# Performance work log

Hardware: AMD Instinct MI355X
Metric: run time of the kernel (lower is better)

The kernel has to match this reference:

```python
import jax, jax.numpy as jnp
import numpy as np
import math

B, S, T = 32, 128, 64
FEAT = 16
H = 1024
V = 32000


def _gru_step(x, h, wih, whh, bih, bhh):
    # torch nn.GRU cell: gates ordered (r, z, n)
    gi = x @ wih.T + bih
    gh = h @ whh.T + bhh
    ir, iz, in_ = jnp.split(gi, 3, axis=-1)
    hr, hz, hn = jnp.split(gh, 3, axis=-1)
    r = jax.nn.sigmoid(ir + hr)
    z = jax.nn.sigmoid(iz + hz)
    n = jnp.tanh(in_ + r * hn)
    return (1.0 - z) * n + z * h


def _forward(features, target_tokens, temp_W, temp_b, hum_W, hum_b, cloud_W, cloud_b,
             time_W, time_b, other_W, other_b, fi_W, fi_b,
             enc_wih, enc_whh, enc_bih, enc_bhh, emb, attn_W, attn_b,
             dec_wih, dec_whh, dec_bih, dec_bhh, out_W, out_b):
    b = features.shape[0]
    # per-feature projections (dropout = identity in eval mode)
    temp = features[:, :, 0:1] @ temp_W.T + temp_b
    hum = features[:, :, 1:2] @ hum_W.T + hum_b
    cloud = features[:, :, 2:3] @ cloud_W.T + cloud_b
    time = features[:, :, -5:-3] @ time_W.T + time_b
    other_in = jnp.concatenate([features[:, :, 3:-5], features[:, :, -3:]], axis=2)
    other = other_in @ other_W.T + other_b
    concat = jnp.concatenate([temp, hum, cloud, time, other], axis=2)  # [B,S,2H]
    proj = jnp.tanh(concat @ fi_W.T + fi_b)  # [B,S,H]

    # encoder GRU over time
    def enc_step(h, x):
        h2 = _gru_step(x, h, enc_wih, enc_whh, enc_bih, enc_bhh)
        return h2, h2
    h0 = jnp.zeros((b, H), proj.dtype)
    h_last, enc_outs = jax.lax.scan(enc_step, h0, proj.transpose(1, 0, 2))
    enc_out = enc_outs.transpose(1, 0, 2)  # [B,S,H]

    # attention keys computed once (loop-invariant in the original)
    keys = enc_out @ attn_W.T + attn_b  # [B,S,H]
    scale = 1.0 / math.sqrt(H)

    # decoder: teacher_forcing_ratio = 1.0 -> input at step t is target_tokens[:, t-1]
    def dec_step(h, tok):
        e = emb[tok]  # [B,H]
        scores = jnp.einsum('bh,bsh->bs', h, keys) * scale
        w = jax.nn.softmax(scores, axis=-1)
        ctx = jnp.einsum('bs,bsh->bh', w, enc_out)
        x = jnp.concatenate([e, ctx], axis=-1)  # [B,2H]
        h2 = _gru_step(x, h, dec_wih, dec_whh, dec_bih, dec_bhh)
        pred = jnp.concatenate([h2, ctx], axis=-1) @ out_W.T + out_b  # [B,V]
        return h2, pred

    _, preds = jax.lax.scan(dec_step, h_last, target_tokens[:, :-1].T)  # [T-1,B,V]
    outputs = jnp.zeros((b, target_tokens.shape[1], V), preds.dtype)
    outputs = outputs.at[:, 0, target_tokens[0, 0]].set(1.0)
    outputs = outputs.at[:, 1:, :].set(preds.transpose(1, 0, 2))
    return outputs


def setup_inputs() -> dict:
    key = jax.random.key(0)
    ks = jax.random.split(key, 32)
    nrm = lambda k, sh: jax.random.normal(k, sh, jnp.float32) * 0.05
    Hq = H // 4
    d = {}
    d['features'] = jax.random.normal(ks[0], (B, S, FEAT), jnp.float32)
    d['target_tokens'] = jax.random.randint(ks[1], (B, T), 0, V, dtype=jnp.int32)
    d['temp_W'] = nrm(ks[2], (Hq, 1)); d['temp_b'] = nrm(ks[3], (Hq,))
    d['hum_W'] = nrm(ks[4], (Hq, 1)); d['hum_b'] = nrm(ks[5], (Hq,))
    d['cloud_W'] = nrm(ks[6], (Hq, 1)); d['cloud_b'] = nrm(ks[7], (Hq,))
    d['time_W'] = nrm(ks[8], (Hq, 2)); d['time_b'] = nrm(ks[9], (Hq,))
    d['other_W'] = nrm(ks[10], (H, FEAT - 5)); d['other_b'] = nrm(ks[11], (H,))
    d['fi_W'] = nrm(ks[12], (H, 2 * H)); d['fi_b'] = nrm(ks[13], (H,))
    d['enc_wih'] = nrm(ks[14], (3 * H, H)); d['enc_whh'] = nrm(ks[15], (3 * H, H))
    d['enc_bih'] = nrm(ks[16], (3 * H,)); d['enc_bhh'] = nrm(ks[17], (3 * H,))
    d['emb'] = nrm(ks[18], (V, H))
    d['attn_W'] = nrm(ks[19], (H, H)); d['attn_b'] = nrm(ks[20], (H,))
    d['dec_wih'] = nrm(ks[21], (3 * H, 2 * H)); d['dec_whh'] = nrm(ks[22], (3 * H, H))
    d['dec_bih'] = nrm(ks[23], (3 * H,)); d['dec_bhh'] = nrm(ks[24], (3 * H,))
    d['out_W'] = nrm(ks[25], (V, 2 * H)); d['out_b'] = nrm(ks[26], (V,))
    return d


def reference(features, target_tokens, temp_W, temp_b, hum_W, hum_b, cloud_W, cloud_b,
              time_W, time_b, other_W, other_b, fi_W, fi_b,
              enc_wih, enc_whh, enc_bih, enc_bhh, emb, attn_W, attn_b,
              dec_wih, dec_whh, dec_bih, dec_bhh, out_W, out_b):
    return _forward(features, target_tokens, temp_W, temp_b, hum_W, hum_b, cloud_W, cloud_b,
                    time_W, time_b, other_W, other_b, fi_W, fi_b,
                    enc_wih, enc_whh, enc_bih, enc_bhh, emb, attn_W, attn_b,
                    dec_wih, dec_whh, dec_bih, dec_bhh, out_W, out_b)
```

## Files before the change

kernel.cpp:

```cpp
#include <hip/hip_runtime.h>

typedef float f32x4 __attribute__((ext_vector_type(4)));
typedef __bf16 bf16x8 __attribute__((ext_vector_type(8)));

#define DI static __device__ __forceinline__

DI unsigned short f2bf(float f) {
  unsigned u = __float_as_uint(f);
  u = (u + 0x7fffu + ((u >> 16) & 1u)) >> 16;
  return (unsigned short)u;
}
DI unsigned pk2(float lo, float hi) {
  return (unsigned)f2bf(lo) | ((unsigned)f2bf(hi) << 16);
}
DI float bflo(unsigned u) { return __uint_as_float(u << 16); }
DI float bfhi(unsigned u) { return __uint_as_float(u & 0xffff0000u); }
DI float sigm(float x) { return 1.0f / (1.0f + expf(-x)); }

DI void gl_lds16(const unsigned short* g, unsigned short* l) {
  __builtin_amdgcn_global_load_lds(
      (const __attribute__((address_space(1))) unsigned int*)g,
      (__attribute__((address_space(3))) unsigned int*)l, 16, 0, 0);
}

DI void st64_sc1(unsigned long long* p, unsigned long long v) {
  __hip_atomic_store(p, v, __ATOMIC_RELAXED, __HIP_MEMORY_SCOPE_AGENT);
}
DI int ldw(const int* p) {
  return __hip_atomic_load(p, __ATOMIC_RELAXED, __HIP_MEMORY_SCOPE_AGENT);
}
DI void stw(int* p, int v) {
  __hip_atomic_store(p, v, __ATOMIC_RELAXED, __HIP_MEMORY_SCOPE_AGENT);
}

DI void burn4(int n) {
  float x0 = 1.f + (float)(int)threadIdx.x, x1 = 2.f, x2 = 3.f, x3 = 4.f;
#pragma unroll 1
  for (int i = 0; i < n; ++i) {
    x0 = __builtin_fmaf(x0, 1.0000001f, 1e-9f);
    x1 = __builtin_fmaf(x1, 1.0000001f, 2e-9f);
    x2 = __builtin_fmaf(x2, 1.0000001f, 3e-9f);
    x3 = __builtin_fmaf(x3, 1.0000001f, 4e-9f);
  }
  asm volatile("" :: "v"(x0), "v"(x1), "v"(x2), "v"(x3));
}

DI void waitrel2(const int* relbase, int repl, int target) {
  const int* w = relbase + repl * 32;
  while (ldw(w) < target) burn4(40);
  asm volatile("" ::: "memory");
}
DI void arrive_release(int* cnt, int nblk, int* relbase, int relval) {
  if (threadIdx.x == 0) {
    int old = __hip_atomic_fetch_add(cnt, 1, __ATOMIC_RELAXED, __HIP_MEMORY_SCOPE_AGENT);
    if (old == nblk - 1) {
#pragma unroll
      for (int i = 0; i < 8; ++i) stw(relbase + i * 32, relval);
    }
  }
}

__global__ void k_fold(const float* __restrict__ tW, const float* __restrict__ tb,
                       const float* __restrict__ hW, const float* __restrict__ hb,
                       const float* __restrict__ cW, const float* __restrict__ cb,
                       const float* __restrict__ tiW, const float* __restrict__ tib,
                       const float* __restrict__ oW, const float* __restrict__ ob,
                       const float* __restrict__ fiW, const float* __restrict__ fib,
                       float* __restrict__ M, float* __restrict__ b0v)
{
  int g = blockIdx.x * 256 + threadIdx.x;
  if (g >= 1024 * 17) return;
  int h = g / 17, f = g - h * 17;
  const float* fw = fiW + (size_t)h * 2048;
  float s = 0.f;
  if (f == 16) {
    for (int k = 0; k < 256; ++k) s += fw[k] * tb[k];
    for (int k = 0; k < 256; ++k) s += fw[256 + k] * hb[k];
    for (int k = 0; k < 256; ++k) s += fw[512 + k] * cb[k];
    for (int k = 0; k < 256; ++k) s += fw[768 + k] * tib[k];
    for (int r = 0; r < 1024; ++r) s += fw[1024 + r] * ob[r];
    b0v[h] = s + fib[h];
  } else if (f == 0) {
    for (int k = 0; k < 256; ++k) s += fw[k] * tW[k];
    M[h * 16 + 0] = s;
  } else if (f == 1) {
    for (int k = 0; k < 256; ++k) s += fw[256 + k] * hW[k];
    M[h * 16 + 1] = s;
  } else if (f == 2) {
    for (int k = 0; k < 256; ++k) s += fw[512 + k] * cW[k];
    M[h * 16 + 2] = s;
// ... 108 lines not shown
    gl_lds16(ga1 + kt, &As[(tid + 256) * 8]);
    gl_lds16(gb0 + kt, &Bs[tid * 8]);
    gl_lds16(gb1 + kt, &Bs[(tid + 256) * 8]);
    __syncthreads();
    bf16x8 af[4], bfv[4];
#pragma unroll
    for (int m = 0; m < 4; ++m) af[m] = *(const bf16x8*)&As[(wm + m * 16 + lr) * 32 + lkb];
#pragma unroll
    for (int n = 0; n < 4; ++n) bfv[n] = *(const bf16x8*)&Bs[(wn + n * 16 + lr) * 32 + lkb];
#pragma unroll
    for (int m = 0; m < 4; ++m)
#pragma unroll
      for (int n = 0; n < 4; ++n)
        acc[m][n] = __builtin_amdgcn_mfma_f32_16x16x32_bf16(af[m], bfv[n], acc[m][n], 0, 0, 0);
  }

#pragma unroll
  for (int m = 0; m < 4; ++m) {
    int rb = tm * 128 + wm + m * 16 + ((lane >> 4) << 2);
#pragma unroll
    for (int n = 0; n < 4; ++n) {
      int c = tn * 128 + wn + n * 16 + lr;
      float bb = bias[c];
#pragma unroll
      for (int i = 0; i < 4; ++i) {
        float v = acc[m][n][i] + bb;
        int r = rb + i;
        if (MODE == 0) {
          Cf[(size_t)r * ldc + c] = v;
        } else if (MODE == 1) {
          Cb[(size_t)r * ldc + c] = f2bf(v);
        } else if (MODE == 3) {
          Cb[(size_t)c * 4096 + r] = f2bf(v);
        } else {
          if (r < 2016) {
            int t = r >> 5, b2 = r & 31;
            Cf[((size_t)b2 * 64 + t + 1) * 32000 + coloff + c] = v;
          }
        }
      }
    }
  }
}

__global__ __launch_bounds__(256, 1)
void k_enc_scan(const float* __restrict__ gi_all, const float* __restrict__ whh,
                const float* __restrict__ bhh, float* __restrict__ hfp,
                unsigned short* __restrict__ enc_bf,
                int* __restrict__ cntE, int* __restrict__ relE)
{
  const int tid = threadIdx.x;
  const int blk = blockIdx.x;

  __shared__ unsigned short W[48 * 1024];
  __shared__ float Cred[4 * 2 * 3 * 64 * 4];
  const int lane = tid & 63, wave = tid >> 6;
  const int j0 = blk * 16;
  const int repl = blk & 7;

  for (int i = tid; i < 48 * 128; i += 256) {
    int r = i >> 7, c = i & 127;
    int gr = ((r >> 4) << 10) + j0 + (r & 15);
    const float* src = whh + ((size_t)gr << 10) + (c << 3);
    f32x4 a = *(const f32x4*)src, b = *(const f32x4*)(src + 4);
    uint4 o;
    o.x = pk2(a[0], a[1]); o.y = pk2(a[2], a[3]);
    o.z = pk2(b[0], b[1]); o.w = pk2(b[2], b[3]);
    *(uint4*)&W[(r << 10) + ((c ^ (r & 7)) << 3)] = o;
  }
  __syncthreads();

// ... 58 lines not shown

    float h2v[2];
#pragma unroll
    for (int cc = 0; cc < 2; ++cc) {
      int lj = clb[cc] + cj[cc], reg = creg[cc], m = cm[cc];
      float Cr = 0.f, Cz = 0.f, Cn = 0.f;
#pragma unroll
      for (int w = 0; w < 4; ++w) {
        Cr += Cred[((((w * 2 + m) * 3 + 0) * 64 + lj) << 2) + reg];
        Cz += Cred[((((w * 2 + m) * 3 + 1) * 64 + lj) << 2) + reg];
        Cn += Cred[((((w * 2 + m) * 3 + 2) * 64 + lj) << 2) + reg];
      }
      float r = sigm(gp[cc][0] + Cr + bh0[cc]);
      float z = sigm(gp[cc][1] + Cz + bh1[cc]);
      float n = tanhf(gp[cc][2] + r * (Cn + bh2[cc]));
      float h2 = (1.f - z) * n + z * hp[cc];
      h2v[cc] = h2; hp[cc] = h2;
    }
    if (s == 127) {
      hfp[cb[0] * 1024 + j0 + cj[0]] = h2v[0];
      hfp[cb[1] * 1024 + j0 + cj[1]] = h2v[1];
    }
#pragma unroll
    for (int cc = 0; cc < 2; ++cc) {
      unsigned short sv = f2bf(h2v[cc]);
      unsigned p = (unsigned)sv | (((unsigned)__shfl_xor((int)(unsigned)sv, 1)) << 16);
      unsigned q = (unsigned)__shfl_xor((int)p, 2);
      if ((tid & 3) == 0) {
        unsigned long long dv = (unsigned long long)p | ((unsigned long long)q << 32);
        st64_sc1((unsigned long long*)&enc_bf[((size_t)cb[cc] * 128 + s) * 1024 + j0 + cj[cc]], dv);
      }
    }
    __syncthreads();
    arrive_release(&cntE[s << 4], 64, relE, s + 1);
  }
}

__global__ __launch_bounds__(256, 1)
void k_dec_scan(const float* __restrict__ gi_e, const float* __restrict__ whh,
                const float* __restrict__ bhh,
                const unsigned short* __restrict__ keys,
                const unsigned short* __restrict__ enc_bf,
                unsigned short* __restrict__ hcat, const float* __restrict__ hfp0,
                const unsigned short* __restrict__ xeT, float* __restrict__ w_all,
                int* __restrict__ cntW, int* __restrict__ cntH,
                int* __restrict__ relDe, int* __restrict__ relDh)
{
  static __shared__ __attribute__((aligned(16))) char smem[135168];
  const int tid = threadIdx.x;
  const int blk = blockIdx.x;
  const int repl = blk & 7;

  if (blk < 64) {
    unsigned short* Ks = (unsigned short*)smem;
    unsigned short* hsh = (unsigned short*)(smem + 131072);
    float* parr = (float*)(smem + 133120);
    const int b = blk >> 1, half = blk & 1;
    const int lane = tid & 63, wave = tid >> 6;

    for (int i = tid; i < 64 * 128; i += 256) {
      int s = i >> 7, c = i & 127;
      uint4 kv = *(const uint4*)(keys + ((size_t)(b * 128 + half * 64 + s) << 10) + (c << 3));
      *(uint4*)&Ks[(s << 10) + ((c ^ (s & 7)) << 3)] = kv;
    }
    __syncthreads();

#pragma unroll 1
    for (int t = 0; t < 63; ++t) {
      if (t) waitrel2(relDh, repl, t);
      const unsigned short* hsrc = (t == 0)
          ? (enc_bf + (size_t)b * 131072 + (size_t)127 * 1024)
          : (hcat + ((size_t)(t - 1) * 32 + b) * 2048);
      *(uint2*)&hsh[tid * 4] = *(const uint2*)(hsrc + tid * 4);
      float a0 = 0.f, a1 = 0.f;
#pragma unroll 8
      for (int i = 0; i < 32; i += 2) {
        int c0 = wave * 32 + i, c1 = c0 + 1;
        uint4 kv0 = *(const uint4*)&Ks[(lane << 10) + ((c0 ^ (lane & 7)) << 3)];
        uint4 kv1 = *(const uint4*)&Ks[(lane << 10) + ((c1 ^ (lane & 7)) << 3)];
        uint4 hv0 = *(const uint4*)&hsh[c0 << 3];
        uint4 hv1 = *(const uint4*)&hsh[c1 << 3];
        a0 += bflo(kv0.x) * bflo(hv0.x) + bfhi(kv0.x) * bfhi(hv0.x)
            + bflo(kv0.y) * bflo(hv0.y) + bfhi(kv0.y) * bfhi(hv0.y)
            + bflo(kv0.z) * bflo(hv0.z) + bfhi(kv0.z) * bfhi(hv0.z)
            + bflo(kv0.w) * bflo(hv0.w) + bfhi(kv0.w) * bfhi(hv0.w);
        a1 += bflo(kv1.x) * bflo(hv1.x) + bfhi(kv1.x) * bfhi(hv1.x)
            + bflo(kv1.y) * bflo(hv1.y) + bfhi(kv1.y) * bfhi(hv1.y)
            + bflo(kv1.z) * bflo(hv1.z) + bfhi(kv1.z) * bfhi(hv1.z)
            + bflo(kv1.w) * bflo(hv1.w) + bfhi(kv1.w) * bfhi(hv1.w);
      }
      parr[wave * 64 + lane] = a0 + a1;
      __syncthreads();
      if (tid < 64) {
        float sc = (parr[tid] + parr[64 + tid] + parr[128 + tid] + parr[192 + tid]) * 0.03125f;
        float e = expf(sc);
        float eo = __shfl_xor(e, 1);
        if ((tid & 1) == 0) {
          unsigned long long dv = (unsigned long long)__float_as_uint(e)
                                | ((unsigned long long)__float_as_uint(eo) << 32);
          st64_sc1((unsigned long long*)(w_all + ((size_t)t * 32 + b) * 128 + half * 64 + tid), dv);
        }
      }
      __syncthreads();
      arrive_release(&cntW[t << 4], 64, relDe, t + 1);
    }
    return;
  }

  unsigned short* Wh = (unsigned short*)smem;
  float* Cred = (float*)(smem + 65536);
  const int lane = tid & 63, wave = tid >> 6;
  const int gblk = blk - 64;
  const int j0 = gblk * 8;

  for (int i = tid; i < 32 * 128; i += 256) {
    int r = i >> 7, c = i & 127;
    int off = (r << 10) + ((c ^ (r & 7)) << 3);
    uint4 oh;
    oh.x = oh.y = oh.z = oh.w = 0u;
    if (r < 24) {
      int gr = ((r >> 3) << 10) + j0 + (r & 7);
      const float* sh = whh + ((size_t)gr << 10) + (c << 3);
      f32x4 a = *(const f32x4*)sh, b = *(const f32x4*)(sh + 4);
      oh.x = pk2(a[0], a[1]); oh.y = pk2(a[2], a[3]);
      oh.z = pk2(b[0], b[1]); oh.w = pk2(b[2], b[3]);
    }
    *(uint4*)&Wh[off] = oh;
  }
  __syncthreads();

  const int gb = tid >> 3, gj = tid & 7;
  const int glb = ((gb & 15) >> 2) * 16;
  const int greg = gb & 3, gm = gb >> 4;
  const float bh0 = bhh[j0 + gj];
  const float bh1 = bhh[1024 + j0 + gj];
  const float bh2 = bhh[2048 + j0 + gj];
  float hpv = hfp0[gb * 1024 + j0 + gj];

  uint4 x0v[16], x1v[16], x2v[16];
  {
    const unsigned short* x0 = xeT + ((size_t)(j0 + gj) << 12) + gb * 128;
    const unsigned short* x1 = xeT + ((size_t)(1024 + j0 + gj) << 12) + gb * 128;
    const unsigned short* x2 = xeT + ((size_t)(2048 + j0 + gj) << 12) + gb * 128;
#pragma unroll
    for (int i = 0; i < 16; ++i) {
      x0v[i] = *(const uint4*)(x0 + i * 8);
      x1v[i] = *(const uint4*)(x1 + i * 8);
      x2v[i] = *(const uint4*)(x2 + i * 8);
    }
  }

#pragma unroll 1
  for (int t = 0; t < 63; ++t) {
    const float* gie = gi_e + ((size_t)t * 32 + gb) * 3072 + j0 + gj;
    float g0 = gie[0], g1 = gie[1024], g2 = gie[2048];

    if (t) waitrel2(relDh, repl, t);
    const unsigned short* abase;
    size_t astr;
    if (t == 0) { abase = enc_bf + (size_t)127 * 1024; astr = 131072; }
    else { abase = hcat + (size_t)(t - 1) * 32 * 2048; astr = 2048; }
    const int k0 = wave << 8;
    f32x4 acc[2][2];
#pragma unroll
    for (int m = 0; m < 2; ++m)
#pragma unroll
      for (int n = 0; n < 2; ++n) { acc[m][n][0]=0.f; acc[m][n][1]=0.f; acc[m][n][2]=0.f; acc[m][n][3]=0.f; }
    {
      bf16x8 af[2][8];
#pragma unroll
      for (int kk = 0; kk < 8; ++kk) {
        int k = k0 + kk * 32 + ((lane >> 4) << 3);
        af[0][kk] = *(const bf16x8*)(abase + (size_t)(lane & 15) * astr + k);
        af[1][kk] = *(const bf16x8*)(abase + (size_t)(16 + (lane & 15)) * astr + k);
      }
#pragma unroll
      for (int kk = 0; kk < 8; ++kk) {
        int c = ((k0 + kk * 32) >> 3) + (lane >> 4);
#pragma unroll
        for (int n = 0; n < 2; ++n) {
          int wr = n * 16 + (lane & 15);
          bf16x8 bfr = *(const bf16x8*)&Wh[(wr << 10) + ((c ^ (wr & 7)) << 3)];
          acc[0][n] = __builtin_amdgcn_mfma_f32_16x16x32_bf16(af[0][kk], bfr, acc[0][n], 0, 0, 0);
          acc[1][n] = __builtin_amdgcn_mfma_f32_16x16x32_bf16(af[1][kk], bfr, acc[1][n], 0, 0, 0);
        }
      }
    }
#pragma unroll
    for (int m = 0; m < 2; ++m)
#pragma unroll
      for (int n = 0; n < 2; ++n)
        *(f32x4*)&Cred[((((wave * 2 + m) * 2 + n) * 64) + lane) << 2] = acc[m][n];
    __syncthreads();

    waitrel2(relDe, repl, t + 1);
    const float* wrow = w_all + ((size_t)t * 32 + gb) * 128;
    float se = 0.f, cx0 = 0.f, cx1 = 0.f, cx2 = 0.f;
#pragma unroll
    for (int i = 0; i < 16; ++i) {
      f32x4 wa = *(const f32x4*)(wrow + i * 8);
      f32x4 wb2 = *(const f32x4*)(wrow + i * 8 + 4);
      se += (wa[0] + wa[1]) + (wa[2] + wa[3]) + (wb2[0] + wb2[1]) + (wb2[2] + wb2[3]);
      uint4 a0 = x0v[i], a1 = x1v[i], a2 = x2v[i];
      cx0 += wa[0]*bflo(a0.x) + wa[1]*bfhi(a0.x) + wa[2]*bflo(a0.y) + wa[3]*bfhi(a0.y)
           + wb2[0]*bflo(a0.z) + wb2[1]*bfhi(a0.z) + wb2[2]*bflo(a0.w) + wb2[3]*bfhi(a0.w);
      cx1 += wa[0]*bflo(a1.x) + wa[1]*bfhi(a1.x) + wa[2]*bflo(a1.y) + wa[3]*bfhi(a1.y)
           + wb2[0]*bflo(a1.z) + wb2[1]*bfhi(a1.z) + wb2[2]*bflo(a1.w) + wb2[3]*bfhi(a1.w);
      cx2 += wa[0]*bflo(a2.x) + wa[1]*bfhi(a2.x) + wa[2]*bflo(a2.y) + wa[3]*bfhi(a2.y)
           + wb2[0]*bflo(a2.z) + wb2[1]*bfhi(a2.z) + wb2[2]*bflo(a2.w) + wb2[3]*bfhi(a2.w);
    }
    float inv = 1.f / se;
    cx0 *= inv; cx1 *= inv; cx2 *= inv;

    {
      float Chr = 0.f, Chz = 0.f, Chn = 0.f;
#pragma unroll
      for (int w = 0; w < 4; ++w) {
        Chr += Cred[((((w * 2 + gm) * 2 + 0) * 64 + glb + gj) << 2) + greg];
        Chz += Cred[((((w * 2 + gm) * 2 + 0) * 64 + glb + gj + 8) << 2) + greg];
        Chn += Cred[((((w * 2 + gm) * 2 + 1) * 64 + glb + gj) << 2) + greg];
      }
      float r = sigm(g0 + cx0 + Chr + bh0);
      float z = sigm(g1 + cx1 + Chz + bh1);
      float n2 = tanhf(g2 + cx2 + r * (Chn + bh2));
      float h2 = (1.f - z) * n2 + z * hpv;
      hpv = h2;
      unsigned short sv = f2bf(h2);
      unsigned p = (unsigned)sv | (((unsigned)__shfl_xor((int)(unsigned)sv, 1)) << 16);
      unsigned q = (unsigned)__shfl_xor((int)p, 2);
      if ((tid & 3) == 0) {
        unsigned long long dv = (unsigned long long)p | ((unsigned long long)q << 32);
        st64_sc1((unsigned long long*)&hcat[((size_t)t * 32 + gb) * 2048 + j0 + gj], dv);
      }
    }
    __syncthreads();
    arrive_release(&cntH[t << 4], 128, relDh, t + 1);
  }
}

__global__ __launch_bounds__(256)
void k_ctx(const float* __restrict__ w_all, const unsigned short* __restrict__ enc_bf,
           unsigned short* __restrict__ hcat)
{
  __shared__ float wsh[8][128];
  __shared__ float inv[8];
  const int b = blockIdx.x, tg = blockIdx.y;
  const int t0 = tg * 8;
  const int nt = (t0 + 8 <= 63) ? 8 : (63 - t0);
  const int tid = threadIdx.x;
  for (int idx = tid; idx < 8 * 128; idx += 256) {
    int tt = idx >> 7, s = idx & 127;
    wsh[tt][s] = (tt < nt) ? w_all[((size_t)(t0 + tt) * 32 + b) * 128 + s] : 0.f;
  }
  __syncthreads();
  if (tid < 8) {
    float s = 0.f;
    for (int i = 0; i < 128; ++i) s += wsh[tid][i];
    inv[tid] = (tid < nt) ? 1.f / s : 0.f;
  }
  __syncthreads();
  const int j0 = tid * 4;
  f32x4 cacc[8];
#pragma unroll
  for (int tt = 0; tt < 8; ++tt) { cacc[tt][0]=0.f; cacc[tt][1]=0.f; cacc[tt][2]=0.f; cacc[tt][3]=0.f; }
  const unsigned short* eb = enc_bf + ((size_t)b << 17) + j0;
  for (int s = 0; s < 128; ++s) {
    uint2 ev = *(const uint2*)(eb + ((size_t)s << 10));
    float v0 = bflo(ev.x), v1 = bfhi(ev.x), v2 = bflo(ev.y), v3 = bfhi(ev.y);
#pragma unroll
    for (int tt = 0; tt < 8; ++tt) {
      float w = wsh[tt][s];
      cacc[tt][0] += w * v0; cacc[tt][1] += w * v1;
      cacc[tt][2] += w * v2; cacc[tt][3] += w * v3;
    }
  }
#pragma unroll
  for (int tt = 0; tt < 8; ++tt) {
    if (tt < nt) {
      float iv = inv[tt];
      uint2 co;
      co.x = pk2(cacc[tt][0] * iv, cacc[tt][1] * iv);
      co.y = pk2(cacc[tt][2] * iv, cacc[tt][3] * iv);
      *(uint2*)(hcat + ((size_t)(t0 + tt) * 32 + b) * 2048 + 1024 + j0) = co;
    }
  }
}

extern "C" void kernel_launch(void* const* d_in, const int* in_sizes, int n_in,
                              void* d_out, int out_size, void* d_ws, size_t ws_size,
                              hipStream_t stream)
{
  const float* features = (const float*)d_in[0];
  const int*   toks     = (const int*)d_in[1];
  const float* temp_W = (const float*)d_in[2];  const float* temp_b = (const float*)d_in[3];
  const float* hum_W  = (const float*)d_in[4];  const float* hum_b  = (const float*)d_in[5];
  const float* cloud_W= (const float*)d_in[6];  const float* cloud_b= (const float*)d_in[7];
  const float* time_W = (const float*)d_in[8];  const float* time_b = (const float*)d_in[9];
  const float* other_W= (const float*)d_in[10]; const float* other_b= (const float*)d_in[11];
  const float* fi_W   = (const float*)d_in[12]; const float* fi_b   = (const float*)d_in[13];
  const float* enc_wih= (const float*)d_in[14]; const float* enc_whh= (const float*)d_in[15];
  const float* enc_bih= (const float*)d_in[16]; const float* enc_bhh= (const float*)d_in[17];
  const float* emb    = (const float*)d_in[18];
  const float* attn_W = (const float*)d_in[19]; const float* attn_b = (const float*)d_in[20];
  const float* dec_wih= (const float*)d_in[21]; const float* dec_whh= (const float*)d_in[22];
  const float* dec_bih= (const float*)d_in[23]; const float* dec_bhh= (const float*)d_in[24];
  const float* out_W  = (const float*)d_in[25]; const float* out_b  = (const float*)d_in[26];
  float* out = (float*)d_out;
  char* ws = (char*)d_ws;

  int*            cntE    = (int*)(ws + 0);
  int*            cntW    = (int*)(ws + 8192);
  int*            cntH    = (int*)(ws + 12288);
  int*            relE    = (int*)(ws + 16384);
  int*            relDe   = (int*)(ws + 17408);
  int*            relDh   = (int*)(ws + 18432);
  float*          zbias   = (float*)(ws + 20480);
  float*          Mf      = (float*)(ws + 32768);
  float*          b0v     = (float*)(ws + 98304);
  float*          hfp     = (float*)(ws + 102400);
  unsigned short* hcat    = (unsigned short*)(ws + 233472);
  unsigned short* keys_bf = (unsigned short*)(ws + 8622080);
  unsigned short* enc_bf  = (unsigned short*)(ws + 17010688);
  float*          w_all   = (float*)(ws + 25399296);
  float*          gi_e    = (float*)(ws + 26447872);
  unsigned short* xeT     = (unsigned short*)(ws + 51613696);
  float*          gi_all  = (float*)(ws + 76779520);
  unsigned short* proj_bf = (unsigned short*)(ws + 127111168);
  unsigned short* e_bf    = (unsigned short*)(ws + 135499776);
  unsigned short* wihE_bf = (unsigned short*)(ws + 139694080);
  unsigned short* attnW_bf= (unsigned short*)(ws + 145985536);
  unsigned short* wihD_bf = (unsigned short*)(ws + 148082688);
  unsigned short* wihDc_bf= (unsigned short*)(ws + 154374144);
  unsigned short* outW_bf = (unsigned short*)(ws + 26447872);

  hipMemsetAsync(ws, 0, 32768, stream);
  hipMemsetAsync(ws + 233472 + (size_t)2016 * 2048 * 2, 0, 32 * 2048 * 2, stream);

  k_conv<<<1536, 256, 0, stream>>>(enc_wih, wihE_bf, 393216);
  k_conv<<<512, 256, 0, stream>>>(attn_W, attnW_bf, 131072);
  k_conv_str<<<3072, 256, 0, stream>>>(dec_wih, wihD_bf, 0);
  k_conv_str<<<3072, 256, 0, stream>>>(dec_wih, wihDc_bf, 1024);

  k_fold<<<68, 256, 0, stream>>>(temp_W, temp_b, hum_W, hum_b, cloud_W, cloud_b,
                                 time_W, time_b, other_W, other_b, fi_W, fi_b, Mf, b0v);
  k_proj<<<dim3(4096, 4), 256, 0, stream>>>(features, Mf, b0v, proj_bf);

  gemm_bf<0><<<768, 256, 0, stream>>>(proj_bf, wihE_bf, enc_bih, gi_all, nullptr,
                                      32, 1024, 1024, 1024, 3072, 0);
  k_enc_scan<<<64, 256, 0, stream>>>(gi_all, enc_whh, enc_bhh, hfp, enc_bf, cntE, relE);

  gemm_bf<1><<<256, 256, 0, stream>>>(enc_bf, attnW_bf, attn_b, nullptr, keys_bf,
                                      32, 1024, 1024, 1024, 1024, 0);
  k_gather_e<<<2048, 256, 0, stream>>>(toks, emb, e_bf);
  gemm_bf<0><<<384, 256, 0, stream>>>(e_bf, wihD_bf, dec_bih, gi_e, nullptr,
                                      16, 1024, 1024, 1024, 3072, 0);
  gemm_bf<3><<<768, 256, 0, stream>>>(enc_bf, wihDc_bf, zbias, nullptr, xeT,
                                      32, 1024, 1024, 1024, 0, 0);
  k_dec_scan<<<192, 256, 0, stream>>>(gi_e, dec_whh, dec_bhh, keys_bf, enc_bf,
                                      hcat, hfp, xeT, w_all, cntW, cntH, relDe, relDh);
  k_ctx<<<dim3(32, 8), 256, 0, stream>>>(w_all, enc_bf, hcat);

  k_conv<<<2048, 256, 0, stream>>>(out_W, outW_bf, 4096000);
  gemm_bf<2><<<2000, 256, 0, stream>>>(hcat, outW_bf, out_b, out, nullptr,
                                       16, 2048, 2048, 2048, 0, 0);
  k_conv<<<2048, 256, 0, stream>>>(out_W + (size_t)16000 * 2048, outW_bf, 4096000);
  gemm_bf<2><<<2000, 256, 0, stream>>>(hcat, outW_bf, out_b + 16000, out, nullptr,
                                       16, 2048, 2048, 2048, 0, 16000);
  k_onehot<<<4000, 256, 0, stream>>>(toks, out);
}
```

Before: 2.752 ms.

## Fuse context and output projection into persistent decoder scan kernel

The decoder scan becomes a persistent kernel with four roles: attention-score blocks (now 128, each handling 32 source positions), GRU hidden-state blocks, per-batch context blocks that write ctx into hcat every step, and output-projection blocks that convert out_W panels to bf16 and run MFMA tiles as soon as the needed timesteps are released. This removes the separate k_ctx, conversion and output GEMM launches and overlaps the large vocab projection with the sequential recurrence. The cost is more release counters and flags (32 replicas), spin-waiting output blocks that compete for CUs, and a dependence on all 413 blocks being co-resident to avoid deadlock.

```diff
diff --git a/kernel.cpp b/kernel.cpp
--- a/kernel.cpp
+++ b/kernel.cpp
@@ -50,12 +50,12 @@
   while (ldw(w) < target) burn4(40);
   asm volatile("" ::: "memory");
 }
-DI void arrive_release(int* cnt, int nblk, int* relbase, int relval) {
+DI void arrive_release(int* cnt, int nblk, int* relbase, int relval, int nrep) {
   if (threadIdx.x == 0) {
     int old = __hip_atomic_fetch_add(cnt, 1, __ATOMIC_RELAXED, __HIP_MEMORY_SCOPE_AGENT);
     if (old == nblk - 1) {
-#pragma unroll
-      for (int i = 0; i < 8; ++i) stw(relbase + i * 32, relval);
+#pragma unroll 1
+      for (int i = 0; i < nrep; ++i) stw(relbase + i * 32, relval);
     }
   }
 }
@@ -230,11 +230,60 @@
           Cb[(size_t)r * ldc + c] = f2bf(v);
         } else if (MODE == 3) {
           Cb[(size_t)c * 4096 + r] = f2bf(v);
-        } else {
-          if (r < 2016) {
-            int t = r >> 5, b2 = r & 31;
-            Cf[((size_t)b2 * 64 + t + 1) * 32000 + coloff + c] = v;
-          }
+        }
+      }
+    }
+  }
+}
+
+DI void out_tile(const unsigned short* A, const unsigned short* Bp,
+                 const float* out_b, float* out, int rowbase, int colbase,
+                 unsigned short* As, unsigned short* Bs, int tid)
+{
+  const int lane = tid & 63, wave = tid >> 6;
+  const int wm = (wave & 1) << 6, wn = (wave >> 1) << 6;
+  const int r0 = tid >> 2, kc0 = (tid & 3) << 3;
+  const unsigned short* ga0 = A + (size_t)r0 * 2048 + kc0;
+  const unsigned short* ga1 = A + (size_t)(64 + r0) * 2048 + kc0;
+  const unsigned short* gb0 = Bp + (size_t)r0 * 2048 + kc0;
+  const unsigned short* gb1 = Bp + (size_t)(64 + r0) * 2048 + kc0;
+  const int lr = lane & 15, lkb = (lane >> 4) << 3;
+  f32x4 acc[4][4];
+#pragma unroll
+  for (int m = 0; m < 4; ++m)
+#pragma unroll
+    for (int n = 0; n < 4; ++n) { acc[m][n][0]=0.f; acc[m][n][1]=0.f; acc[m][n][2]=0.f; acc[m][n][3]=0.f; }
+  for (int kt = 0; kt < 2048; kt += 32) {
+    __syncthreads();
+    gl_lds16(ga0 + kt, &As[tid * 8]);
+    gl_lds16(ga1 + kt, &As[(tid + 256) * 8]);
+    gl_lds16(gb0 + kt, &Bs[tid * 8]);
+    gl_lds16(gb1 + kt, &Bs[(tid + 256) * 8]);
+    __syncthreads();
+    bf16x8 af[4], bfv[4];
+#pragma unroll
+    for (int m = 0; m < 4; ++m) af[m] = *(const bf16x8*)&As[(wm + m * 16 + lr) * 32 + lkb];
+#pragma unroll
+    for (int n = 0; n < 4; ++n) bfv[n] = *(const bf16x8*)&Bs[(wn + n * 16 + lr) * 32 + lkb];
+#pragma unroll
+    for (int m = 0; m < 4; ++m)
+#pragma unroll
+      for (int n = 0; n < 4; ++n)
+        acc[m][n] = __builtin_amdgcn_mfma_f32_16x16x32_bf16(af[m], bfv[n], acc[m][n], 0, 0, 0);
+  }
+#pragma unroll
+  for (int m = 0; m < 4; ++m) {
+    int rb = rowbase + wm + m * 16 + ((lane >> 4) << 2);
+#pragma unroll
+    for (int n = 0; n < 4; ++n) {
+      int cg = colbase + wn + n * 16 + lr;
+      float bb = out_b[cg];
+#pragma unroll
+      for (int i = 0; i < 4; ++i) {
+        int r = rb + i;
+        if (r < 2016) {
+          int t = r >> 5, b2 = r & 31;
+          out[((size_t)b2 * 64 + t + 1) * 32000 + cg] = acc[m][n][i] + bb;
         }
       }
     }
@@ -359,7 +408,7 @@
       }
     }
     __syncthreads();
-    arrive_release(&cntE[s << 4], 64, relE, s + 1);
+    arrive_release(&cntE[s << 4], 64, relE, s + 1, 8);
   }
 }
 
@@ -370,25 +419,29 @@
                 const unsigned short* __restrict__ enc_bf,
                 unsigned short* __restrict__ hcat, const float* __restrict__ hfp0,
                 const unsigned short* __restrict__ xeT, float* __restrict__ w_all,
-                int* __restrict__ cntW, int* __restrict__ cntH,
-                int* __restrict__ relDe, int* __restrict__ relDh)
-{
-  static __shared__ __attribute__((aligned(16))) char smem[135168];
+                int* __restrict__ cntW, int* __restrict__ cntH, int* __restrict__ cntC,
+                int* __restrict__ relDe, int* __restrict__ relDh, int* __restrict__ relCtx,
+                const float* __restrict__ out_W, const float* __restrict__ out_b,
+                unsigned short* __restrict__ outWp, float* __restrict__ out)
+{
+  static __shared__ __attribute__((aligned(16))) char smem[81920];
   const int tid = threadIdx.x;
   const int blk = blockIdx.x;
-  const int repl = blk & 7;
-
-  if (blk < 64) {
+  const int repl = blk & 31;
+
+  if (blk < 128) {
     unsigned short* Ks = (unsigned short*)smem;
-    unsigned short* hsh = (unsigned short*)(smem + 131072);
-    float* parr = (float*)(smem + 133120);
-    const int b = blk >> 1, half = blk & 1;
+    unsigned short* hsh = (unsigned short*)(smem + 65536);
+    float* parr = (float*)(smem + 67584);
+    const int b = blk >> 2, q = blk & 3;
     const int lane = tid & 63, wave = tid >> 6;
-
-    for (int i = tid; i < 64 * 128; i += 256) {
-      int s = i >> 7, c = i & 127;
-      uint4 kv = *(const uint4*)(keys + ((size_t)(b * 128 + half * 64 + s) << 10) + (c << 3));
-      *(uint4*)&Ks[(s << 10) + ((c ^ (s & 7)) << 3)] = kv;
+    const int s = lane & 31;
+    const int ksl = (wave << 1) | (lane >> 5);
+
+    for (int i = tid; i < 32 * 128; i += 256) {
+      int sr = i >> 7, c = i & 127;
+      uint4 kv = *(const uint4*)(keys + ((size_t)(b * 128 + q * 32 + sr) << 10) + (c << 3));
+      *(uint4*)&Ks[(sr << 10) + ((c ^ (sr & 15)) << 3)] = kv;
     }
     __syncthreads();
 
@@ -399,12 +452,13 @@
           ? (enc_bf + (size_t)b * 131072 + (size_t)127 * 1024)
           : (hcat + ((size_t)(t - 1) * 32 + b) * 2048);
       *(uint2*)&hsh[tid * 4] = *(const uint2*)(hsrc + tid * 4);
+      __syncthreads();
       float a0 = 0.f, a1 = 0.f;
-#pragma unroll 8
-      for (int i = 0; i < 32; i += 2) {
-        int c0 = wave * 32 + i, c1 = c0 + 1;
-        uint4 kv0 = *(const uint4*)&Ks[(lane << 10) + ((c0 ^ (lane & 7)) << 3)];
-        uint4 kv1 = *(const uint4*)&Ks[(lane << 10) + ((c1 ^ (lane & 7)) << 3)];
+#pragma unroll
+      for (int i = 0; i < 16; i += 2) {
+        int c0 = (ksl << 4) + i, c1 = c0 + 1;
+        uint4 kv0 = *(const uint4*)&Ks[(s << 10) + ((c0 ^ (s & 15)) << 3)];
+        uint4 kv1 = *(const uint4*)&Ks[(s << 10) + ((c1 ^ (s & 15)) << 3)];
         uint4 hv0 = *(const uint4*)&hsh[c0 << 3];
         uint4 hv1 = *(const uint4*)&hsh[c1 << 3];
         a0 += bflo(kv0.x) * bflo(hv0.x) + bfhi(kv0.x) * bfhi(hv0.x)
@@ -416,199 +470,217 @@
             + bflo(kv1.z) * bflo(hv1.z) + bfhi(kv1.z) * bfhi(hv1.z)
             + bflo(kv1.w) * bflo(hv1.w) + bfhi(kv1.w) * bfhi(hv1.w);
       }
-      parr[wave * 64 + lane] = a0 + a1;
-      __syncthreads();
-      if (tid < 64) {
-        float sc = (parr[tid] + parr[64 + tid] + parr[128 + tid] + parr[192 + tid]) * 0.03125f;
-        float e = expf(sc);
+      parr[(ksl << 5) + s] = a0 + a1;
+      __syncthreads();
+      if (tid < 32) {
+        float sc = 0.f;
+#pragma unroll
+        for (int k = 0; k < 8; ++k) sc += parr[(k << 5) + tid];
+        float e = expf(sc * 0.03125f);
         float eo = __shfl_xor(e, 1);
         if ((tid & 1) == 0) {
           unsigned long long dv = (unsigned long long)__float_as_uint(e)
                                 | ((unsigned long long)__float_as_uint(eo) << 32);
-          st64_sc1((unsigned long long*)(w_all + ((size_t)t * 32 + b) * 128 + half * 64 + tid), dv);
+          st64_sc1((unsigned long long*)(w_all + ((size_t)t * 32 + b) * 128 + q * 32 + tid), dv);
         }
       }
       __syncthreads();
-      arrive_release(&cntW[t << 4], 64, relDe, t + 1);
+      arrive_release(&cntW[t << 4], 128, relDe, t + 1, 32);
     }
     return;
   }
 
-  unsigned short* Wh = (unsigned short*)smem;
-  float* Cred = (float*)(smem + 65536);
-  const int lane = tid & 63, wave = tid >> 6;
-  const int gblk = blk - 64;
-  const int j0 = gblk * 8;
-
-  for (int i = tid; i < 32 * 128; i += 256) {
-    int r = i >> 7, c = i & 127;
-    int off = (r << 10) + ((c ^ (r & 7)) << 3);
-    uint4 oh;
-    oh.x = oh.y = oh.z = oh.w = 0u;
-    if (r < 24) {
-      int gr = ((r >> 3) << 10) + j0 + (r & 7);
-      const float* sh = whh + ((size_t)gr << 10) + (c << 3);
-      f32x4 a = *(const f32x4*)sh, b = *(const f32x4*)(sh + 4);
-      oh.x = pk2(a[0], a[1]); oh.y = pk2(a[2], a[3]);
-      oh.z = pk2(b[0], b[1]); oh.w = pk2(b[2], b[3]);
-    }
-    *(uint4*)&Wh[off] = oh;
-  }
-  __syncthreads();
-
-  const int gb = tid >> 3, gj = tid & 7;
-  const int glb = ((gb & 15) >> 2) * 16;
-  const int greg = gb & 3, gm = gb >> 4;
-  const float bh0 = bhh[j0 + gj];
-  const float bh1 = bhh[1024 + j0 + gj];
-  const float bh2 = bhh[2048 + j0 + gj];
-  float hpv = hfp0[gb * 1024 + j0 + gj];
-
-  uint4 x0v[16], x1v[16], x2v[16];
+  if (blk < 256) {
+    unsigned short* Wh = (unsigned short*)smem;
+    float* Cred = (float*)(smem + 65536);
+    const int lane = tid & 63, wave = tid >> 6;
+    const int gblk = blk - 128;
+    const int j0 = gblk * 8;
+
+    for (int i = tid; i < 32 * 128; i += 256) {
+      int r = i >> 7, c = i & 127;
+      int off = (r << 10) + ((c ^ (r & 7)) << 3);
+      uint4 oh;
+      oh.x = oh.y = oh.z = oh.w = 0u;
+      if (r < 24) {
+        int gr = ((r >> 3) << 10) + j0 + (r & 7);
+        const float* sh = whh + ((size_t)gr << 10) + (c << 3);
+        f32x4 a = *(const f32x4*)sh, b = *(const f32x4*)(sh + 4);
+        oh.x = pk2(a[0], a[1]); oh.y = pk2(a[2], a[3]);
+        oh.z = pk2(b[0], b[1]); oh.w = pk2(b[2], b[3]);
+      }
+      *(uint4*)&Wh[off] = oh;
+    }
+    __syncthreads();
+
+    const int gb = tid >> 3, gj = tid & 7;
+    const int glb = ((gb & 15) >> 2) * 16;
+    const int greg = gb & 3, gm = gb >> 4;
+    const float bh0 = bhh[j0 + gj];
+    const float bh1 = bhh[1024 + j0 + gj];
+    const float bh2 = bhh[2048 + j0 + gj];
+    float hpv = hfp0[gb * 1024 + j0 + gj];
+
+    uint4 x0v[16], x1v[16], x2v[16];
+    {
+      const unsigned short* x0 = xeT + ((size_t)(j0 + gj) << 12) + gb * 128;
+      const unsigned short* x1 = xeT + ((size_t)(1024 + j0 + gj) << 12) + gb * 128;
+      const unsigned short* x2 = xeT + ((size_t)(2048 + j0 + gj) << 12) + gb * 128;
+#pragma unroll
+      for (int i = 0; i < 16; ++i) {
+        x0v[i] = *(const uint4*)(x0 + i * 8);
+        x1v[i] = *(const uint4*)(x1 + i * 8);
+        x2v[i] = *(const uint4*)(x2 + i * 8);
+      }
+    }
+
+#pragma unroll 1
+    for (int t = 0; t < 63; ++t) {
+      const float* gie = gi_e + ((size_t)t * 32 + gb) * 3072 + j0 + gj;
+      float g0 = gie[0], g1 = gie[1024], g2 = gie[2048];
+
+      if (t) waitrel2(relDh, repl, t);
+      const unsigned short* abase;
+      size_t astr;
+      if (t == 0) { abase = enc_bf + (size_t)127 * 1024; astr = 131072; }
+      else { abase = hcat + (size_t)(t - 1) * 32 * 2048; astr = 2048; }
+      const int k0 = wave << 8;
+      f32x4 acc[2][2];
+#pragma unroll
+      for (int m = 0; m < 2; ++m)
+#pragma unroll
+        for (int n = 0; n < 2; ++n) { acc[m][n][0]=0.f; acc[m][n][1]=0.f; acc[m][n][2]=0.f; acc[m][n][3]=0.f; }
+      {
+        bf16x8 af[2][8];
+#pragma unroll
+        for (int kk = 0; kk < 8; ++kk) {
+          int k = k0 + kk * 32 + ((lane >> 4) << 3);
+          af[0][kk] = *(const bf16x8*)(abase + (size_t)(lane & 15) * astr + k);
+          af[1][kk] = *(const bf16x8*)(abase + (size_t)(16 + (lane & 15)) * astr + k);
+        }
+#pragma unroll
+        for (int kk = 0; kk < 8; ++kk) {
+          int c = ((k0 + kk * 32) >> 3) + (lane >> 4);
+#pragma unroll
+          for (int n = 0; n < 2; ++n) {
+            int wr = n * 16 + (lane & 15);
+            bf16x8 bfr = *(const bf16x8*)&Wh[(wr << 10) + ((c ^ (wr & 7)) << 3)];
+            acc[0][n] = __builtin_amdgcn_mfma_f32_16x16x32_bf16(af[0][kk], bfr, acc[0][n], 0, 0, 0);
+            acc[1][n] = __builtin_amdgcn_mfma_f32_16x16x32_bf16(af[1][kk], bfr, acc[1][n], 0, 0, 0);
+          }
+        }
+      }
+#pragma unroll
+      for (int m = 0; m < 2; ++m)
+#pragma unroll
+        for (int n = 0; n < 2; ++n)
+          *(f32x4*)&Cred[((((wave * 2 + m) * 2 + n) * 64) + lane) << 2] = acc[m][n];
+      __syncthreads();
+
+      waitrel2(relDe, repl, t + 1);
+      const float* wrow = w_all + ((size_t)t * 32 + gb) * 128;
+      float se = 0.f, cx0 = 0.f, cx1 = 0.f, cx2 = 0.f;
+#pragma unroll
+      for (int i = 0; i < 16; ++i) {
+        f32x4 wa = *(const f32x4*)(wrow + i * 8);
+        f32x4 wb2 = *(const f32x4*)(wrow + i * 8 + 4);
+        se += (wa[0] + wa[1]) + (wa[2] + wa[3]) + (wb2[0] + wb2[1]) + (wb2[2] + wb2[3]);
+        uint4 a0 = x0v[i], a1 = x1v[i], a2 = x2v[i];
+        cx0 += wa[0]*bflo(a0.x) + wa[1]*bfhi(a0.x) + wa[2]*bflo(a0.y) + wa[3]*bfhi(a0.y)
+             + wb2[0]*bflo(a0.z) + wb2[1]*bfhi(a0.z) + wb2[2]*bflo(a0.w) + wb2[3]*bfhi(a0.w);
+        cx1 += wa[0]*bflo(a1.x) + wa[1]*bfhi(a1.x) + wa[2]*bflo(a1.y) + wa[3]*bfhi(a1.y)
+             + wb2[0]*bflo(a1.z) + wb2[1]*bfhi(a1.z) + wb2[2]*bflo(a1.w) + wb2[3]*bfhi(a1.w);
+        cx2 += wa[0]*bflo(a2.x) + wa[1]*bfhi(a2.x) + wa[2]*bflo(a2.y) + wa[3]*bfhi(a2.y)
+             + wb2[0]*bflo(a2.z) + wb2[1]*bfhi(a2.z) + wb2[2]*bflo(a2.w) + wb2[3]*bfhi(a2.w);
+      }
+      float inv = 1.f / se;
+      cx0 *= inv; cx1 *= inv; cx2 *= inv;
+
+      {
+        float Chr = 0.f, Chz = 0.f, Chn = 0.f;
+#pragma unroll
+        for (int w = 0; w < 4; ++w) {
+          Chr += Cred[((((w * 2 + gm) * 2 + 0) * 64 + glb + gj) << 2) + greg];
+          Chz += Cred[((((w * 2 + gm) * 2 + 0) * 64 + glb + gj + 8) << 2) + greg];
+          Chn += Cred[((((w * 2 + gm) * 2 + 1) * 64 + glb + gj) << 2) + greg];
+        }
+        float r = sigm(g0 + cx0 + Chr + bh0);
+        float z = sigm(g1 + cx1 + Chz + bh1);
+        float n2 = tanhf(g2 + cx2 + r * (Chn + bh2));
+        float h2 = (1.f - z) * n2 + z * hpv;
+        hpv = h2;
+        unsigned short sv = f2bf(h2);
+        unsigned p = (unsigned)sv | (((unsigned)__shfl_xor((int)(unsigned)sv, 1)) << 16);
+        unsigned qq = (unsigned)__shfl_xor((int)p, 2);
+        if ((tid & 3) == 0) {
+          unsigned long long dv = (unsigned long long)p | ((unsigned long long)qq << 32);
+          st64_sc1((unsigned long long*)&hcat[((size_t)t * 32 + gb) * 2048 + j0 + gj], dv);
+        }
+      }
+      __syncthreads();
+      arrive_release(&cntH[t << 4], 128, relDh, t + 1, 32);
+    }
+    return;
+  }
+
+  if (blk < 288) {
+    float* wsh = (float*)smem;
+    const int b = blk - 256;
+#pragma unroll 1
+    for (int t = 0; t < 63; ++t) {
+      waitrel2(relDe, repl, t + 1);
+      if (tid < 32)
+        *(f32x4*)&wsh[tid * 4] = *(const f32x4*)(w_all + ((size_t)t * 32 + b) * 128 + tid * 4);
+      __syncthreads();
+      float se = 0.f;
+#pragma unroll
+      for (int i = 0; i < 128; i += 4) se += (wsh[i] + wsh[i+1]) + (wsh[i+2] + wsh[i+3]);
+      float inv = 1.f / se;
+      const int j0 = tid * 4;
+      f32x4 cacc; cacc[0]=0.f; cacc[1]=0.f; cacc[2]=0.f; cacc[3]=0.f;
+      const unsigned short* eb = enc_bf + ((size_t)b << 17) + j0;
+      for (int s2 = 0; s2 < 128; ++s2) {
+        float w = wsh[s2];
+        uint2 ev = *(const uint2*)(eb + ((size_t)s2 << 10));
+        cacc[0] += w * bflo(ev.x); cacc[1] += w * bfhi(ev.x);
+        cacc[2] += w * bflo(ev.y); cacc[3] += w * bfhi(ev.y);
+      }
+      unsigned long long cw = (unsigned long long)pk2(cacc[0] * inv, cacc[1] * inv)
+                            | ((unsigned long long)pk2(cacc[2] * inv, cacc[3] * inv) << 32);
+      st64_sc1((unsigned long long*)(hcat + ((size_t)t * 32 + b) * 2048 + 1024 + j0), cw);
+      __syncthreads();
+      arrive_release(&cntC[t << 4], 32, relCtx, t + 1, 32);
+    }
+    return;
+  }
+
   {
-    const unsigned short* x0 = xeT + ((size_t)(j0 + gj) << 12) + gb * 128;
-    const unsigned short* x1 = xeT + ((size_t)(1024 + j0 + gj) << 12) + gb * 128;
-    const unsigned short* x2 = xeT + ((size_t)(2048 + j0 + gj) << 12) + gb * 128;
-#pragma unroll
-    for (int i = 0; i < 16; ++i) {
-      x0v[i] = *(const uint4*)(x0 + i * 8);
-      x1v[i] = *(const uint4*)(x1 + i * 8);
-      x2v[i] = *(const uint4*)(x2 + i * 8);
-    }
-  }
-
+    unsigned short* As = (unsigned short*)smem;
+    unsigned short* Bs = (unsigned short*)(smem + 8192);
+    const int tn = blk - 288;
+    unsigned short* panel = outWp + (size_t)tn * 262144;
 #pragma unroll 1
-  for (int t = 0; t < 63; ++t) {
-    const float* gie = gi_e + ((size_t)t * 32 + gb) * 3072 + j0 + gj;
-    float g0 = gie[0], g1 = gie[1024], g2 = gie[2048];
-
-    if (t) waitrel2(relDh, repl, t);
-    const unsigned short* abase;
-    size_t astr;
-    if (t == 0) { abase = enc_bf + (size_t)127 * 1024; astr = 131072; }
-    else { abase = hcat + (size_t)(t - 1) * 32 * 2048; astr = 2048; }
-    const int k0 = wave << 8;
-    f32x4 acc[2][2];
-#pragma unroll
-    for (int m = 0; m < 2; ++m)
-#pragma unroll
-      for (int n = 0; n < 2; ++n) { acc[m][n][0]=0.f; acc[m][n][1]=0.f; acc[m][n][2]=0.f; acc[m][n][3]=0.f; }
-    {
-      bf16x8 af[2][8];
-#pragma unroll
-      for (int kk = 0; kk < 8; ++kk) {
-        int k = k0 + kk * 32 + ((lane >> 4) << 3);
-        af[0][kk] = *(const bf16x8*)(abase + (size_t)(lane & 15) * astr + k);
-        af[1][kk] = *(const bf16x8*)(abase + (size_t)(16 + (lane & 15)) * astr + k);
-      }
-#pragma unroll
-      for (int kk = 0; kk < 8; ++kk) {
-        int c = ((k0 + kk * 32) >> 3) + (lane >> 4);
-#pragma unroll
-        for (int n = 0; n < 2; ++n) {
-          int wr = n * 16 + (lane & 15);
-          bf16x8 bfr = *(const bf16x8*)&Wh[(wr << 10) + ((c ^ (wr & 7)) << 3)];
-          acc[0][n] = __builtin_amdgcn_mfma_f32_16x16x32_bf16(af[0][kk], bfr, acc[0][n], 0, 0, 0);
-          acc[1][n] = __builtin_amdgcn_mfma_f32_16x16x32_bf16(af[1][kk], bfr, acc[1][n], 0, 0, 0);
-        }
-      }
-    }
-#pragma unroll
-    for (int m = 0; m < 2; ++m)
-#pragma unroll
-      for (int n = 0; n < 2; ++n)
-        *(f32x4*)&Cred[((((wave * 2 + m) * 2 + n) * 64) + lane) << 2] = acc[m][n];
-    __syncthreads();
-
-    waitrel2(relDe, repl, t + 1);
-    const float* wrow = w_all + ((size_t)t * 32 + gb) * 128;
-    float se = 0.f, cx0 = 0.f, cx1 = 0.f, cx2 = 0.f;
-#pragma unroll
-    for (int i = 0; i < 16; ++i) {
-      f32x4 wa = *(const f32x4*)(wrow + i * 8);
-      f32x4 wb2 = *(const f32x4*)(wrow + i * 8 + 4);
-      se += (wa[0] + wa[1]) + (wa[2] + wa[3]) + (wb2[0] + wb2[1]) + (wb2[2] + wb2[3]);
-      uint4 a0 = x0v[i], a1 = x1v[i], a2 = x2v[i];
-      cx0 += wa[0]*bflo(a0.x) + wa[1]*bfhi(a0.x) + wa[2]*bflo(a0.y) + wa[3]*bfhi(a0.y)
-           + wb2[0]*bflo(a0.z) + wb2[1]*bfhi(a0.z) + wb2[2]*bflo(a0.w) + wb2[3]*bfhi(a0.w);
-      cx1 += wa[0]*bflo(a1.x) + wa[1]*bfhi(a1.x) + wa[2]*bflo(a1.y) + wa[3]*bfhi(a1.y)
-           + wb2[0]*bflo(a1.z) + wb2[1]*bfhi(a1.z) + wb2[2]*bflo(a1.w) + wb2[3]*bfhi(a1.w);
-      cx2 += wa[0]*bflo(a2.x) + wa[1]*bfhi(a2.x) + wa[2]*bflo(a2.y) + wa[3]*bfhi(a2.y)
-           + wb2[0]*bflo(a2.z) + wb2[1]*bfhi(a2.z) + wb2[2]*bflo(a2.w) + wb2[3]*bfhi(a2.w);
-    }
-    float inv = 1.f / se;
-    cx0 *= inv; cx1 *= inv; cx2 *= inv;
-
-    {
-      float Chr = 0.f, Chz = 0.f, Chn = 0.f;
-#pragma unroll
-      for (int w = 0; w < 4; ++w) {
-        Chr += Cred[((((w * 2 + gm) * 2 + 0) * 64 + glb + gj) << 2) + greg];
-        Chz += Cred[((((w * 2 + gm) * 2 + 0) * 64 + glb + gj + 8) << 2) + greg];
-        Chn += Cred[((((w * 2 + gm) * 2 + 1) * 64 + glb + gj) << 2) + greg];
-      }
-      float r = sigm(g0 + cx0 + Chr + bh0);
-      float z = sigm(g1 + cx1 + Chz + bh1);
-      float n2 = tanhf(g2 + cx2 + r * (Chn + bh2));
-      float h2 = (1.f - z) * n2 + z * hpv;
-      hpv = h2;
-      unsigned short sv = f2bf(h2);
-      unsigned p = (unsigned)sv | (((unsigned)__shfl_xor((int)(unsigned)sv, 1)) << 16);
-      unsigned q = (unsigned)__shfl_xor((int)p, 2);
-      if ((tid & 3) == 0) {
-        unsigned long long dv = (unsigned long long)p | ((unsigned long long)q << 32);
-        st64_sc1((unsigned long long*)&hcat[((size_t)t * 32 + gb) * 2048 + j0 + gj], dv);
-      }
-    }
-    __syncthreads();
-    arrive_release(&cntH[t << 4], 128, relDh, t + 1);
-  }
-}
-
-__global__ __launch_bounds__(256)
-void k_ctx(const float* __restrict__ w_all, const unsigned short* __restrict__ enc_bf,
-           unsigned short* __restrict__ hcat)
-{
-  __shared__ float wsh[8][128];
-  __shared__ float inv[8];
-  const int b = blockIdx.x, tg = blockIdx.y;
-  const int t0 = tg * 8;
-  const int nt = (t0 + 8 <= 63) ? 8 : (63 - t0);
-  const int tid = threadIdx.x;
-  for (int idx = tid; idx < 8 * 128; idx += 256) {
-    int tt = idx >> 7, s = idx & 127;
-    wsh[tt][s] = (tt < nt) ? w_all[((size_t)(t0 + tt) * 32 + b) * 128 + s] : 0.f;
-  }
-  __syncthreads();
-  if (tid < 8) {
-    float s = 0.f;
-    for (int i = 0; i < 128; ++i) s += wsh[tid][i];
-    inv[tid] = (tid < nt) ? 1.f / s : 0.f;
-  }
-  __syncthreads();
-  const int j0 = tid * 4;
-  f32x4 cacc[8];
-#pragma unroll
-  for (int tt = 0; tt < 8; ++tt) { cacc[tt][0]=0.f; cacc[tt][1]=0.f; cacc[tt][2]=0.f; cacc[tt][3]=0.f; }
-  const unsigned short* eb = enc_bf + ((size_t)b << 17) + j0;
-  for (int s = 0; s < 128; ++s) {
-    uint2 ev = *(const uint2*)(eb + ((size_t)s << 10));
-    float v0 = bflo(ev.x), v1 = bfhi(ev.x), v2 = bflo(ev.y), v3 = bfhi(ev.y);
-#pragma unroll
-    for (int tt = 0; tt < 8; ++tt) {
-      float w = wsh[tt][s];
-      cacc[tt][0] += w * v0; cacc[tt][1] += w * v1;
-      cacc[tt][2] += w * v2; cacc[tt][3] += w * v3;
-    }
-  }
-#pragma unroll
-  for (int tt = 0; tt < 8; ++tt) {
-    if (tt < nt) {
-      float iv = inv[tt];
-      uint2 co;
-      co.x = pk2(cacc[tt][0] * iv, cacc[tt][1] * iv);
-      co.y = pk2(cacc[tt][2] * iv, cacc[tt][3] * iv);
-      *(uint2*)(hcat + ((size_t)(t0 + tt) * 32 + b) * 2048 + 1024 + j0) = co;
+    for (int half = 0; half < 2; ++half) {
+      const int coloff = half * 16000;
+      const float* src = out_W + (size_t)(coloff + tn * 128) * 2048;
+      for (int i = tid; i < 32768; i += 256) {
+        const float* p = src + (size_t)i * 8;
+        f32x4 a = *(const f32x4*)p, b = *(const f32x4*)(p + 4);
+        uint4 o;
+        o.x = pk2(a[0], a[1]); o.y = pk2(a[2], a[3]);
+        o.z = pk2(b[0], b[1]); o.w = pk2(b[2], b[3]);
+        *(uint4*)(panel + (size_t)i * 8) = o;
+      }
+      __syncthreads();
+#pragma unroll 1
+      for (int tm = 0; tm < 16; ++tm) {
+        int gate = 4 * tm + 4; if (gate > 63) gate = 63;
+        waitrel2(relDh, repl, gate);
+        waitrel2(relCtx, repl, gate);
+        out_tile(hcat + (size_t)tm * 128 * 2048, panel, out_b, out,
+                 tm * 128, coloff + tn * 128, As, Bs, tid);
+      }
+      __syncthreads();
     }
   }
 }
@@ -635,33 +707,35 @@
   float* out = (float*)d_out;
   char* ws = (char*)d_ws;
 
-  int*            cntE    = (int*)(ws + 0);
-  int*            cntW    = (int*)(ws + 8192);
-  int*            cntH    = (int*)(ws + 12288);
-  int*            relE    = (int*)(ws + 16384);
-  int*            relDe   = (int*)(ws + 17408);
-  int*            relDh   = (int*)(ws + 18432);
-  float*          zbias   = (float*)(ws + 20480);
-  float*          Mf      = (float*)(ws + 32768);
-  float*          b0v     = (float*)(ws + 98304);
-  float*          hfp     = (float*)(ws + 102400);
-  unsigned short* hcat    = (unsigned short*)(ws + 233472);
-  unsigned short* keys_bf = (unsigned short*)(ws + 8622080);
-  unsigned short* enc_bf  = (unsigned short*)(ws + 17010688);
-  float*          w_all   = (float*)(ws + 25399296);
-  float*          gi_e    = (float*)(ws + 26447872);
-  unsigned short* xeT     = (unsigned short*)(ws + 51613696);
-  float*          gi_all  = (float*)(ws + 76779520);
-  unsigned short* proj_bf = (unsigned short*)(ws + 127111168);
-  unsigned short* e_bf    = (unsigned short*)(ws + 135499776);
-  unsigned short* wihE_bf = (unsigned short*)(ws + 139694080);
-  unsigned short* attnW_bf= (unsigned short*)(ws + 145985536);
-  unsigned short* wihD_bf = (unsigned short*)(ws + 148082688);
-  unsigned short* wihDc_bf= (unsigned short*)(ws + 154374144);
-  unsigned short* outW_bf = (unsigned short*)(ws + 26447872);
-
-  hipMemsetAsync(ws, 0, 32768, stream);
-  hipMemsetAsync(ws + 233472 + (size_t)2016 * 2048 * 2, 0, 32 * 2048 * 2, stream);
+  int*            cntW    = (int*)(ws + 0);
+  int*            cntH    = (int*)(ws + 4096);
+  int*            cntC    = (int*)(ws + 8192);
+  int*            cntE    = (int*)(ws + 12288);
+  int*            relE    = (int*)(ws + 20480);
+  int*            relDe   = (int*)(ws + 24576);
+  int*            relDh   = (int*)(ws + 28672);
+  int*            relCtx  = (int*)(ws + 32768);
+  float*          zbias   = (float*)(ws + 40960);
+  float*          Mf      = (float*)(ws + 65536);
+  float*          b0v     = (float*)(ws + 131072);
+  float*          hfp     = (float*)(ws + 135168);
+  unsigned short* hcat    = (unsigned short*)(ws + 266240);
+  unsigned short* keys_bf = (unsigned short*)(ws + 8654848);
+  unsigned short* enc_bf  = (unsigned short*)(ws + 17043456);
+  float*          w_all   = (float*)(ws + 25432064);
+  float*          gi_e    = (float*)(ws + 26464256);
+  unsigned short* xeT     = (unsigned short*)(ws + 51236864);
+  unsigned short* wihE_bf = (unsigned short*)(ws + 76402688);
+  unsigned short* attnW_bf= (unsigned short*)(ws + 82694144);
+  unsigned short* wihD_bf = (unsigned short*)(ws + 84791296);
+  unsigned short* wihDc_bf= (unsigned short*)(ws + 91082752);
+  unsigned short* proj_bf = (unsigned short*)(ws + 97374208);
+  unsigned short* e_bf    = (unsigned short*)(ws + 105762816);
+  float*          gi_all  = (float*)(ws + 109957120);
+  unsigned short* outWp   = (unsigned short*)(ws + 76402688);
+
+  hipMemsetAsync(ws, 0, 53248, stream);
+  hipMemsetAsync(ws + 266240 + (size_t)2016 * 2048 * 2, 0, 32 * 2048 * 2, stream);
 
   k_conv<<<1536, 256, 0, stream>>>(enc_wih, wihE_bf, 393216);
   k_conv<<<512, 256, 0, stream>>>(attn_W, attnW_bf, 131072);
@@ -683,15 +757,9 @@
                                       16, 1024, 1024, 1024, 3072, 0);
   gemm_bf<3><<<768, 256, 0, stream>>>(enc_bf, wihDc_bf, zbias, nullptr, xeT,
                                       32, 1024, 1024, 1024, 0, 0);
-  k_dec_scan<<<192, 256, 0, stream>>>(gi_e, dec_whh, dec_bhh, keys_bf, enc_bf,
-                                      hcat, hfp, xeT, w_all, cntW, cntH, relDe, relDh);
-  k_ctx<<<dim3(32, 8), 256, 0, stream>>>(w_all, enc_bf, hcat);
-
-  k_conv<<<2048, 256, 0, stream>>>(out_W, outW_bf, 4096000);
-  gemm_bf<2><<<2000, 256, 0, stream>>>(hcat, outW_bf, out_b, out, nullptr,
-                                       16, 2048, 2048, 2048, 0, 0);
-  k_conv<<<2048, 256, 0, stream>>>(out_W + (size_t)16000 * 2048, outW_bf, 4096000);
-  gemm_bf<2><<<2000, 256, 0, stream>>>(hcat, outW_bf, out_b + 16000, out, nullptr,
-                                       16, 2048, 2048, 2048, 0, 16000);
+  k_dec_scan<<<413, 256, 0, stream>>>(gi_e, dec_whh, dec_bhh, keys_bf, enc_bf,
+                                      hcat, hfp, xeT, w_all,
+                                      cntW, cntH, cntC, relDe, relDh, relCtx,
+                                      out_W, out_b, outWp, out);
   k_onehot<<<4000, 256, 0, stream>>>(toks, out);
 }
```

New measurement: 3.808 ms. +38.4%, slower.
